# Performance work log

Hardware: AMD Instinct MI355X
Metric: run time of the kernel (lower is better)

The kernel has to match this reference:

```python
import jax, jax.numpy as jnp
import numpy as np

V, E, H2, TAG = 32000, 128, 256, 9
H = H2 // 2          # per-direction LSTM hidden
B, T = 128, 512


def setup_inputs() -> dict:
    key = jax.random.key(0)
    ks = jax.random.split(key, 15)
    s = 0.08
    n = lambda k, shp: jax.random.normal(k, shp, dtype=jnp.float32) * s
    return {
        "sentence": jax.random.randint(ks[0], (B, T), 0, V, dtype=jnp.int32),
        "tags": jax.random.randint(ks[1], (B, T), 0, TAG, dtype=jnp.int32),
        "mask": jnp.ones((B, T), dtype=bool),
        "embedding": n(ks[2], (V, E)),
        "w_ih_f": n(ks[3], (4 * H, E)),
        "w_hh_f": n(ks[4], (4 * H, H)),
        "b_f": n(ks[5], (4 * H,)),
        "w_ih_b": n(ks[6], (4 * H, E)),
        "w_hh_b": n(ks[7], (4 * H, H)),
        "b_b": n(ks[8], (4 * H,)),
        "w_out": n(ks[9], (TAG, H2)),
        "b_out": n(ks[10], (TAG,)),
        "start_trans": n(ks[11], (TAG,)),
        "end_trans": n(ks[12], (TAG,)),
        "trans": n(ks[13], (TAG, TAG)),
    }


def _lstm_dir(xp, w_hh):
    """xp: [T,B,4H] precomputed input projections (incl. bias). Returns h seq [T,B,H]."""
    Hn = w_hh.shape[1]
    Bn = xp.shape[1]

    def step(carry, x_t):
        h, c = carry
        g = x_t + h @ w_hh.T                       # [B,4H]
        i, f, gg, o = jnp.split(g, 4, axis=-1)     # torch gate order: i,f,g,o
        c = jax.nn.sigmoid(f) * c + jax.nn.sigmoid(i) * jnp.tanh(gg)
        h = jax.nn.sigmoid(o) * jnp.tanh(c)
        return (h, c), h

    init = (jnp.zeros((Bn, Hn), xp.dtype), jnp.zeros((Bn, Hn), xp.dtype))
    _, hs = jax.lax.scan(step, init, xp)
    return hs


def reference(sentence, tags, mask, embedding, w_ih_f, w_hh_f, b_f,
              w_ih_b, w_hh_b, b_b, w_out, b_out, start_trans, end_trans, trans):
    # ---- BiLSTM emissions ----
    x = embedding[sentence]                 # [B,T,E]
    xt = jnp.swapaxes(x, 0, 1)              # [T,B,E]
    h_f = _lstm_dir(xt @ w_ih_f.T + b_f, w_hh_f)                 # [T,B,H]
    h_b = _lstm_dir((xt @ w_ih_b.T + b_b)[::-1], w_hh_b)[::-1]   # [T,B,H]
    hcat = jnp.concatenate([h_f, h_b], axis=-1)                  # [T,B,2H]
    emissions = hcat @ w_out.T + b_out                           # [T,B,TAG]

    m = mask.T.astype(emissions.dtype)      # [T,B]
    tt = tags.T                             # [T,B]
    bidx = jnp.arange(tt.shape[1])

    # ---- CRF numerator (score of gold path), torchcrf semantics ----
    num0 = start_trans[tt[0]] + emissions[0, bidx, tt[0]]        # [B]

    def num_step(score, inp):
        e_t, t_prev, t_cur, m_t = inp
        return score + (trans[t_prev, t_cur] + e_t[bidx, t_cur]) * m_t, None

    num, _ = jax.lax.scan(num_step, num0, (emissions[1:], tt[:-1], tt[1:], m[1:]))
    seq_ends = mask.sum(axis=1).astype(jnp.int32) - 1            # [B]
    last_tags = tt[seq_ends, bidx]
    num = num + end_trans[last_tags]

    # ---- CRF log-partition (forward algorithm) ----
    alpha0 = start_trans + emissions[0]                          # [B,TAG]

    def fwd_step(alpha, inp):
        e_t, m_t = inp
        nxt = jax.nn.logsumexp(alpha[:, :, None] + trans[None] + e_t[:, None, :], axis=1)
        return jnp.where(m_t[:, None] > 0, nxt, alpha), None

    alpha, _ = jax.lax.scan(fwd_step, alpha0, (emissions[1:], m[1:]))
    logZ = jax.nn.logsumexp(alpha + end_trans, axis=1)           # [B]

    # forward returns -crf(...) with reduction='mean' => mean negative log-likelihood
    return -jnp.mean(num - logZ)
```

## Files before the change

kernel.cpp:

```cpp
#include <hip/hip_runtime.h>
#include <hip/hip_bf16.h>
#include <cstdint>
#include <cstddef>

#define NB   128
#define NT   512
#define NE   128
#define NH   128
#define NG   512
#define NTAG 9

typedef __bf16 bf16;
typedef __bf16 bf16x4 __attribute__((ext_vector_type(4)));
typedef __bf16 bf16x8 __attribute__((ext_vector_type(8)));
typedef _Float16 f16;
typedef _Float16 f16x2 __attribute__((ext_vector_type(2)));
typedef _Float16 f16x8 __attribute__((ext_vector_type(8)));
typedef float  floatx4 __attribute__((ext_vector_type(4)));

__device__ __forceinline__ float bflo_f32(unsigned u) {
  union { unsigned x; float f; } c; c.x = u << 16; return c.f;
}
__device__ __forceinline__ float bfhi_f32(unsigned u) {
  union { unsigned x; float f; } c; c.x = u & 0xFFFF0000u; return c.f;
}
__device__ __forceinline__ f16x2 pkh(float a, float b) {
  return __builtin_bit_cast(f16x2, __builtin_amdgcn_cvt_pkrtz(a, b));
}
__device__ __forceinline__ void block_sync_lds() {
  asm volatile("s_waitcnt lgkmcnt(0)\n\ts_barrier" ::: "memory");
}

__device__ __forceinline__ f16x2 sigm_h(f16x2 x) {
  const f16x2 lo = {(f16)(-2.5f), (f16)(-2.5f)}, hi = {(f16)2.5f, (f16)2.5f};
  x = __builtin_elementwise_min(__builtin_elementwise_max(x, lo), hi);
  f16x2 t = x * x;
  f16x2 p = t * (f16)0.0010154f + (f16)(-0.019144f);
  p = t * p + (f16)0.24964f;
  return x * p + (f16)0.5f;
}
__device__ __forceinline__ f16x2 tanh_h(f16x2 x) {
  const f16x2 lo = {(f16)(-1.5f), (f16)(-1.5f)}, hi = {(f16)1.5f, (f16)1.5f};
  x = __builtin_elementwise_min(__builtin_elementwise_max(x, lo), hi);
  f16x2 t = x * x;
  f16x2 p = t * (f16)0.045172f + (f16)(-0.27334f);
  p = t * p + (f16)0.98976f;
  return x * p;
}

__global__ __launch_bounds__(256, 1) void k_xp(
    const int* __restrict__ sentence, const float* __restrict__ emb,
    const float* __restrict__ w_ih_f, const float* __restrict__ w_ih_b,
    const float* __restrict__ b_f, const float* __restrict__ b_b,
    bf16* __restrict__ xp_f, bf16* __restrict__ xp_b)
{
  __shared__ bf16 Cld[128 * 136];
  const int t = blockIdx.x;
  const int tid = threadIdx.x;
  const int wv = tid >> 6, lane = tid & 63;
  const int lrow = lane & 15, quad = lane >> 4;
  const int m0 = (wv & 1) * 64, n0 = (wv >> 1) * 64;

  int tokv[4];
  #pragma unroll
  for (int mt = 0; mt < 4; ++mt)
    tokv[mt] = sentence[(size_t)(m0 + mt * 16 + lrow) * NT + t];

  bf16x8 af[4][4];
  #pragma unroll
  for (int kk = 0; kk < 4; ++kk)
    #pragma unroll
    for (int mt = 0; mt < 4; ++mt) {
      const float* s = emb + (size_t)tokv[mt] * NE + kk * 32 + quad * 8;
      float4 lo = *(const float4*)s;
      float4 hi = *(const float4*)(s + 4);
      bf16x8 v;
      v[0] = (bf16)lo.x; v[1] = (bf16)lo.y; v[2] = (bf16)lo.z; v[3] = (bf16)lo.w;
      v[4] = (bf16)hi.x; v[5] = (bf16)hi.y; v[6] = (bf16)hi.z; v[7] = (bf16)hi.w;
      af[kk][mt] = v;
    }

  bool first = true;
  #pragma unroll
  for (int d = 0; d < 2; ++d) {
    const float* Wd       = d ? w_ih_b : w_ih_f;
    const float* biasbase = d ? b_b  : b_f;
    bf16* outdir          = d ? xp_b : xp_f;
    for (int nb = 0; nb < 4; ++nb) {
      const int colbase = nb * 128;

      floatx4 acc[4][4] = {};
      #pragma unroll
      for (int kk = 0; kk < 4; ++kk) {
        bf16x8 bfr[4];
        #pragma unroll
        for (int nt = 0; nt < 4; ++nt) {
          const float* s = Wd + (size_t)(colbase + n0 + nt * 16 + lrow) * 128 + kk * 32 + quad * 8;
          float4 lo = *(const float4*)s;
          float4 hi = *(const float4*)(s + 4);
          bf16x8 v;
          v[0] = (bf16)lo.x; v[1] = (bf16)lo.y; v[2] = (bf16)lo.z; v[3] = (bf16)lo.w;
          v[4] = (bf16)hi.x; v[5] = (bf16)hi.y; v[6] = (bf16)hi.z; v[7] = (bf16)hi.w;
          bfr[nt] = v;
        }
        #pragma unroll
        for (int mt = 0; mt < 4; ++mt)
          #pragma unroll
          for (int nt = 0; nt < 4; ++nt)
            acc[mt][nt] = __builtin_amdgcn_mfma_f32_16x16x32_bf16(af[kk][mt], bfr[nt], acc[mt][nt], 0, 0, 0);
      }
      float bv[4];
      #pragma unroll
      for (int nt = 0; nt < 4; ++nt) bv[nt] = biasbase[colbase + n0 + nt * 16 + lrow];

      if (!first) __syncthreads();
      first = false;
      #pragma unroll
      for (int mt = 0; mt < 4; ++mt)
        #pragma unroll
        for (int nt = 0; nt < 4; ++nt) {
          bf16x4 v4;
          #pragma unroll
          for (int rr = 0; rr < 4; ++rr) v4[rr] = (bf16)(acc[mt][nt][rr] + bv[nt]);
          *(bf16x4*)&Cld[(n0 + nt * 16 + lrow) * 136 + m0 + mt * 16 + quad * 4] = v4;
        }
      __syncthreads();
      bf16* outbase = outdir + ((size_t)t * 8) * (512 * 16) + (size_t)colbase * 16;
      #pragma unroll
      for (int it = 0; it < 8; ++it) {
        const int p = it * 256 + tid;
        const int bg = p >> 8, n = (p >> 1) & 127, half = p & 1;
        *(bf16x8*)(outbase + ((size_t)bg * 512 + n) * 16 + half * 8) =
            *(const bf16x8*)&Cld[n * 136 + bg * 16 + half * 8];
      }
    }
  }
}

#define LSTM_STEP(PX, RB, WB)                                                  \
  do {                                                                         \
    f16x8 af[4];                                                               \
    _Pragma("unroll")                                                          \
    for (int kk = 0; kk < 4; ++kk)                                             \
      af[kk] = *(const f16x8*)&(RB)[lane * 8 + kk * 512];                      \
    floatx4 acc[4];                                                            \
    _Pragma("unroll")                                                          \
    for (int g = 0; g < 4; ++g) {                                              \
      acc[g][0] = bflo_f32(PX[g][0]); acc[g][1] = bfhi_f32(PX[g][0]);          \
      acc[g][2] = bflo_f32(PX[g][1]); acc[g][3] = bfhi_f32(PX[g][1]);          \
    }                                                                          \
    _Pragma("unroll")                                                          \
    for (int g = 0; g < 4; ++g) {             \
      uint2 u = *(const uint2*)pg[g];                                          \
      PX[g][0] = u.x; PX[g][1] = u.y;                                          \
      pg[g] += dstep_x;                                                        \
    }                                                                          \
    _Pragma("unroll")                                                          \
    for (int kk = 0; kk < 4; ++kk)                                             \
      _Pragma("unroll")                                                        \
      for (int g = 0; g < 4; ++g)                                              \
        acc[g] = __builtin_amdgcn_mfma_f32_16x16x32_f16(af[kk], wf[g][kk],     \
                                                        acc[g], 0, 0, 0);      \
    {                                                                          \
      f16x2 iv, fv, gv, ov, h2;                                                \
      iv = sigm_h(pkh(acc[0][0], acc[0][1]));                                  \
      fv = sigm_h(pkh(acc[1][0], acc[1][1]));                                  \
      gv = tanh_h(pkh(acc[2][0], acc[2][1]));                                  \
      ov = sigm_h(pkh(acc[3][0], acc[3][1]));                                  \
      c01 = fv * c01 + iv * gv;                                                \
      h2 = ov * tanh_h(c01);                                                   \
      (WB)[wboff + 0 * 8] = h2[0]; (WB)[wboff + 1 * 8] = h2[1];                \
      hop[0 * NH] = h2[0]; hop[1 * NH] = h2[1];                                \
      iv = sigm_h(pkh(acc[0][2], acc[0][3]));                                  \
      fv = sigm_h(pkh(acc[1][2], acc[1][3]));                                  \
      gv = tanh_h(pkh(acc[2][2], acc[2][3]));                                  \
      ov = sigm_h(pkh(acc[3][2], acc[3][3]));                                  \
      c23 = fv * c23 + iv * gv;                                                \
      h2 = ov * tanh_h(c23);                                                   \
      (WB)[wboff + 2 * 8] = h2[0]; (WB)[wboff + 3 * 8] = h2[1];                \
      hop[2 * NH] = h2[0]; hop[3 * NH] = h2[1];                                \
    }                                                                          \
    hop += dstep_h;                                                            \
    block_sync_lds();                                                          \
  } while (0)

__global__ __launch_bounds__(512, 1) void k_lstm(
    const bf16* __restrict__ xp_f, const bf16* __restrict__ xp_b,
    const float* __restrict__ w_hh_f, const float* __restrict__ w_hh_b,
    f16* __restrict__ h_f, f16* __restrict__ h_b)
{
  __shared__ f16 hfrag[2][2048];
  const int wg = blockIdx.x;
  const int dir = wg >> 3;
  const int bb = wg & 7;
  const int b0 = bb * 16;
  const bf16* __restrict__ xp   = dir ? xp_b   : xp_f;
  const float* __restrict__ Whh = dir ? w_hh_b : w_hh_f;
  f16* __restrict__ hout        = dir ? h_b    : h_f;
  const int tid = threadIdx.x;
  const int wv = tid >> 6, lane = tid & 63;
  const int lrow = lane & 15, quad = lane >> 4;
  const int hc = wv * 16 + lrow;

  f16x8 wf[4][4];
  #pragma unroll
  for (int g = 0; g < 4; ++g)
    #pragma unroll
    for (int kk = 0; kk < 4; ++kk) {
      const float* src = Whh + (size_t)(g * 128 + hc) * 128 + kk * 32 + quad * 8;
      f16x8 v;
      #pragma unroll
      for (int j = 0; j < 8; ++j) v[j] = (f16)src[j];
      wf[g][kk] = v;
    }
  {
    f16x2 z = {(f16)0.f, (f16)0.f};
    *(f16x2*)&hfrag[0][tid * 2] = z;
    *(f16x2*)&hfrag[0][1024 + tid * 2] = z;
  }

  const int t0 = dir ? (NT - 1) : 0;
  const ptrdiff_t dstep_x = dir ? -(ptrdiff_t)(8 * 512 * 16) : (ptrdiff_t)(8 * 512 * 16);
  const ptrdiff_t dstep_h = dir ? -(ptrdiff_t)(NB * NH) : (ptrdiff_t)(NB * NH);

  const bf16* pg[4];
  unsigned pxA[4][2], pxB[4][2];
  #pragma unroll
  for (int g = 0; g < 4; ++g)
    pg[g] = xp + (((size_t)t0 * 8 + bb) * 512 + g * 128 + hc) * 16 + quad * 4;
  #pragma unroll
  for (int g = 0; g < 4; ++g) {
    uint2 u = *(const uint2*)pg[g];
    pxA[g][0] = u.x; pxA[g][1] = u.y;
    pg[g] += dstep_x;
  }
  #pragma unroll
  for (int g = 0; g < 4; ++g) {
    uint2 u = *(const uint2*)pg[g];
    pxB[g][0] = u.x; pxB[g][1] = u.y;
    pg[g] += dstep_x;
  }
  f16* hop = hout + ((size_t)t0 * NB + b0 + quad * 4) * NH + hc;
  const int wboff = ((hc >> 3) * 16 + quad * 4) * 8 + (hc & 7);
  f16x2 c01 = {(f16)0.f, (f16)0.f}, c23 = {(f16)0.f, (f16)0.f};
  block_sync_lds();

  for (int s = 0; s < NT; s += 2) {
    LSTM_STEP(pxA, hfrag[0], hfrag[1]);
    LSTM_STEP(pxB, hfrag[1], hfrag[0]);
  }
}

__global__ __launch_bounds__(256, 1) void k_emis(
    const f16* __restrict__ h_f, const f16* __restrict__ h_b,
    const float* __restrict__ w_out, const float* __restrict__ b_out,
    float* __restrict__ emis, int* __restrict__ cnt_all)
{
  const int tid = threadIdx.x;
  if (blockIdx.x == 0 && tid == 0) *cnt_all = 0;
  const int wv = tid >> 6, lane = tid & 63;
  const int lrow = lane & 15, quad = lane >> 4;
  const int m0 = blockIdx.x * 64 + wv * 16;
  const size_t mrow = (size_t)(m0 + lrow);

  f16x8 wo[8];
  #pragma unroll
  for (int kk = 0; kk < 8; ++kk) {
    f16x8 v;
    #pragma unroll
    for (int j = 0; j < 8; ++j) v[j] = (f16)0.0f;
    if (lrow < NTAG) {
      const float* src = w_out + (size_t)lrow * 256 + kk * 32 + quad * 8;
      #pragma unroll
      for (int j = 0; j < 8; ++j) v[j] = (f16)src[j];
    }
    wo[kk] = v;
  }
  floatx4 acc = {};
  #pragma unroll
  for (int kk = 0; kk < 4; ++kk) {
    const f16x8 a = *(const f16x8*)&h_f[mrow * NH + kk * 32 + quad * 8];
    acc = __builtin_amdgcn_mfma_f32_16x16x32_f16(a, wo[kk], acc, 0, 0, 0);
  }
  #pragma unroll
  for (int kk = 0; kk < 4; ++kk) {
    const f16x8 a = *(const f16x8*)&h_b[mrow * NH + kk * 32 + quad * 8];
    acc = __builtin_amdgcn_mfma_f32_16x16x32_f16(a, wo[kk + 4], acc, 0, 0, 0);
  }
  if (lrow < NTAG) {
    const float bb = b_out[lrow];
    #pragma unroll
    for (int rr = 0; rr < 4; ++rr)
      emis[(size_t)(m0 + quad * 4 + rr) * NTAG + lrow] = acc[rr] + bb;
  }
}

__global__ __launch_bounds__(576, 1) void k_crf(
    const float* __restrict__ emis, const float* __restrict__ trans,
    const int* __restrict__ tags, const float* __restrict__ start_trans,
    const float* __restrict__ end_trans, float* __restrict__ res,
    int* __restrict__ cnt_all, float* __restrict__ out)
{
  __shared__ float Pl[64 * 81];
  __shared__ float nred[8];
  __shared__ int s_last;
  const int b = blockIdx.x;
  const int tid = threadIdx.x;

  float T[81];
  #pragma unroll
  for (int k = 0; k < 81; ++k) T[k] = trans[k];

  {
    const int c = tid / 9;
    const int i = tid - c * 9;
    const int t1 = 1 + 8 * c;
    const int nst = (c == 63) ? 6 : 7;
    const float* erow = emis + ((size_t)t1 * NB + b) * NTAG;
    float alpha[9];
    #pragma unroll
    for (int j = 0; j < 9; ++j) alpha[j] = trans[i * 9 + j] + erow[j];
    for (int tt = 0; tt < nst; ++tt) {
      erow += NB * NTAG;
      float e[9];
      #pragma unroll
      for (int j = 0; j < 9; ++j) e[j] = erow[j];
      float na[9];
      #pragma unroll
      for (int j = 0; j < 9; ++j) {
        float m = alpha[0] + T[0 * 9 + j];
        #pragma unroll
        for (int k = 1; k < 9; ++k) m = fmaxf(m, alpha[k] + T[k * 9 + j]);
        float s = 0.0f;
        #pragma unroll
        for (int k = 0; k < 9; ++k) s += __expf(alpha[k] + T[k * 9 + j] - m);
        na[j] = m + __logf(s) + e[j];
      }
      #pragma unroll
      for (int j = 0; j < 9; ++j) alpha[j] = na[j];
    }
    #pragma unroll
    for (int j = 0; j < 9; ++j) Pl[c * 81 + i * 9 + j] = alpha[j];
  }

  if (tid < 512) {
    float nval;
    if (tid == 0) {
      const int tg0 = tags[b * NT];
      const int tgl = tags[b * NT + NT - 1];
      nval = start_trans[tg0] + emis[b * NTAG + tg0] + end_trans[tgl];
    } else {
      const int tp = tags[b * NT + tid - 1];
      const int tc = tags[b * NT + tid];
      nval = trans[tp * NTAG + tc] + emis[(tid * NB + b) * NTAG + tc];
    }
    #pragma unroll
    for (int m = 32; m >= 1; m >>= 1) nval += __shfl_xor(nval, m, 64);
    if ((tid & 63) == 0) nred[tid >> 6] = nval;
  }
  __syncthreads();

  #pragma unroll
  for (int sp = 1; sp < 64; sp <<= 1) {
    const int nprod = 32 / sp;
    if (tid < nprod * 9) {
      const int p = tid / 9, i2 = tid - p * 9;
      const int c0 = p * 2 * sp;
      float Arow[9];
      #pragma unroll
      for (int k = 0; k < 9; ++k) Arow[k] = Pl[c0 * 81 + i2 * 9 + k];
      const float* Bm = &Pl[(c0 + sp) * 81];
      float Crow[9];
      #pragma unroll
      for (int j = 0; j < 9; ++j) {
        float m = Arow[0] + Bm[0 * 9 + j];
        #pragma unroll
        for (int k = 1; k < 9; ++k) m = fmaxf(m, Arow[k] + Bm[k * 9 + j]);
        float s = 0.0f;
        #pragma unroll
        for (int k = 0; k < 9; ++k) s += __expf(Arow[k] + Bm[k * 9 + j] - m);
        Crow[j] = m + __logf(s);
      }
      #pragma unroll
      for (int j = 0; j < 9; ++j) Pl[c0 * 81 + i2 * 9 + j] = Crow[j];
    }
    __syncthreads();
  }

  if (tid == 0) {
    float a0[9];
    #pragma unroll
    for (int j = 0; j < 9; ++j) a0[j] = start_trans[j] + emis[b * NTAG + j];
    float av[9];
    #pragma unroll
    for (int j = 0; j < 9; ++j) {
      float m = a0[0] + Pl[0 * 9 + j];
      #pragma unroll
      for (int k = 1; k < 9; ++k) m = fmaxf(m, a0[k] + Pl[k * 9 + j]);
      float s = 0.0f;
      #pragma unroll
      for (int k = 0; k < 9; ++k) s += __expf(a0[k] + Pl[k * 9 + j] - m);
      av[j] = m + __logf(s) + end_trans[j];
    }
    float m2 = av[0];
    #pragma unroll
    for (int k = 1; k < 9; ++k) m2 = fmaxf(m2, av[k]);
    float s2 = 0.0f;
    #pragma unroll
    for (int k = 0; k < 9; ++k) s2 += __expf(av[k] - m2);
    const float logZ = m2 + __logf(s2);
    float nsum = 0.0f;
    #pragma unroll
    for (int w = 0; w < 8; ++w) nsum += nred[w];
    res[b] = logZ - nsum;
  }

  if (tid == 0) {
    __threadfence();
    s_last = (atomicAdd(cnt_all, 1) == NB - 1) ? 1 : 0;
  }
  __syncthreads();
  if (!s_last) return;
  __threadfence();
  if (tid < 128) {
    float v = res[tid];
    #pragma unroll
    for (int m = 32; m >= 1; m >>= 1) v += __shfl_xor(v, m, 64);
    if ((tid & 63) == 0) nred[tid >> 6] = v;
  }
  __syncthreads();
  if (tid == 0) out[0] = (nred[0] + nred[1]) * (1.0f / 128.0f);
}

extern "C" void kernel_launch(void* const* d_in, const int* in_sizes, int n_in,
                              void* d_out, int out_size, void* d_ws, size_t ws_size,
                              hipStream_t stream)
{
  (void)in_sizes; (void)n_in; (void)out_size; (void)ws_size;
  const int*   sentence    = (const int*)d_in[0];
  const int*   tags        = (const int*)d_in[1];
  const float* embedding   = (const float*)d_in[3];
  const float* w_ih_f      = (const float*)d_in[4];
  const float* w_hh_f      = (const float*)d_in[5];
  const float* b_f         = (const float*)d_in[6];
  const float* w_ih_b      = (const float*)d_in[7];
  const float* w_hh_b      = (const float*)d_in[8];
  const float* b_b         = (const float*)d_in[9];
  const float* w_out       = (const float*)d_in[10];
  const float* b_out       = (const float*)d_in[11];
  const float* start_trans = (const float*)d_in[12];
  const float* end_trans   = (const float*)d_in[13];
  const float* trans       = (const float*)d_in[14];
  float* out = (float*)d_out;

  char* ws = (char*)d_ws;
  bf16*  xp_f = (bf16*)(ws);
  bf16*  xp_b = (bf16*)(ws + 67108864);
  f16*   h_f  = (f16*)(ws + 134217728);
  f16*   h_b  = (f16*)(ws + 150994944);
  float* emis = (float*)(ws + 167772160);
  float* res   = (float*)(ws + 136871936);
  int*   cnt_all = (int*)(ws);

  k_xp<<<512, 256, 0, stream>>>(sentence, embedding, w_ih_f, w_ih_b,
                                b_f, b_b, xp_f, xp_b);
  k_lstm<<<16, 512, 0, stream>>>(xp_f, xp_b, w_hh_f, w_hh_b, h_f, h_b);
  k_emis<<<1024, 256, 0, stream>>>(h_f, h_b, w_out, b_out, emis, cnt_all);
  k_crf<<<128, 576, 0, stream>>>(emis, trans, tags, start_trans, end_trans,
                                 res, cnt_all, out);
}
```

Baseline: 564.5 us.

## Fuse emission projection into CRF kernel with per-batch emissions in LDS

Removes the separate emission kernel. Each CRF block now computes its own batch row's emissions with MFMA from the LSTM hidden states and stores them in shared memory, instead of reading them from a global buffer. The counter reset moves to the xp kernel and the workspace offsets are rearranged. This saves a kernel launch and a global round trip for the emissions. In exchange, the CRF blocks take on strided hidden-state reads spread over only 128 blocks, and the larger shared-memory footprint may limit occupancy.

```diff
diff --git a/kernel.cpp b/kernel.cpp
--- a/kernel.cpp
+++ b/kernel.cpp
@@ -52,11 +52,12 @@
     const int* __restrict__ sentence, const float* __restrict__ emb,
     const float* __restrict__ w_ih_f, const float* __restrict__ w_ih_b,
     const float* __restrict__ b_f, const float* __restrict__ b_b,
-    bf16* __restrict__ xp_f, bf16* __restrict__ xp_b)
+    bf16* __restrict__ xp_f, bf16* __restrict__ xp_b, int* __restrict__ cnt_all)
 {
   __shared__ bf16 Cld[128 * 136];
   const int t = blockIdx.x;
   const int tid = threadIdx.x;
+  if (t == 0 && tid == 0) *cnt_all = 0;
   const int wv = tid >> 6, lane = tid & 63;
   const int lrow = lane & 15, quad = lane >> 4;
   const int m0 = (wv & 1) * 64, n0 = (wv >> 1) * 64;
@@ -251,61 +252,58 @@
   }
 }
 
-__global__ __launch_bounds__(256, 1) void k_emis(
+__global__ __launch_bounds__(576, 1) void k_crf(
     const f16* __restrict__ h_f, const f16* __restrict__ h_b,
     const float* __restrict__ w_out, const float* __restrict__ b_out,
-    float* __restrict__ emis, int* __restrict__ cnt_all)
+    const float* __restrict__ trans, const int* __restrict__ tags,
+    const float* __restrict__ start_trans, const float* __restrict__ end_trans,
+    float* __restrict__ res, int* __restrict__ cnt_all, float* __restrict__ out)
 {
-  const int tid = threadIdx.x;
-  if (blockIdx.x == 0 && tid == 0) *cnt_all = 0;
-  const int wv = tid >> 6, lane = tid & 63;
-  const int lrow = lane & 15, quad = lane >> 4;
-  const int m0 = blockIdx.x * 64 + wv * 16;
-  const size_t mrow = (size_t)(m0 + lrow);
-
-  f16x8 wo[8];
-  #pragma unroll
-  for (int kk = 0; kk < 8; ++kk) {
-    f16x8 v;
-    #pragma unroll
-    for (int j = 0; j < 8; ++j) v[j] = (f16)0.0f;
-    if (lrow < NTAG) {
-      const float* src = w_out + (size_t)lrow * 256 + kk * 32 + quad * 8;
-      #pragma unroll
-      for (int j = 0; j < 8; ++j) v[j] = (f16)src[j];
-    }
-    wo[kk] = v;
-  }
-  floatx4 acc = {};
-  #pragma unroll
-  for (int kk = 0; kk < 4; ++kk) {
-    const f16x8 a = *(const f16x8*)&h_f[mrow * NH + kk * 32 + quad * 8];
-    acc = __builtin_amdgcn_mfma_f32_16x16x32_f16(a, wo[kk], acc, 0, 0, 0);
-  }
-  #pragma unroll
-  for (int kk = 0; kk < 4; ++kk) {
-    const f16x8 a = *(const f16x8*)&h_b[mrow * NH + kk * 32 + quad * 8];
-    acc = __builtin_amdgcn_mfma_f32_16x16x32_f16(a, wo[kk + 4], acc, 0, 0, 0);
-  }
-  if (lrow < NTAG) {
-    const float bb = b_out[lrow];
-    #pragma unroll
-    for (int rr = 0; rr < 4; ++rr)
-      emis[(size_t)(m0 + quad * 4 + rr) * NTAG + lrow] = acc[rr] + bb;
-  }
-}
-
-__global__ __launch_bounds__(576, 1) void k_crf(
-    const float* __restrict__ emis, const float* __restrict__ trans,
-    const int* __restrict__ tags, const float* __restrict__ start_trans,
-    const float* __restrict__ end_trans, float* __restrict__ res,
-    int* __restrict__ cnt_all, float* __restrict__ out)
-{
+  __shared__ float emisL[NT * NTAG];
   __shared__ float Pl[64 * 81];
   __shared__ float nred[8];
   __shared__ int s_last;
   const int b = blockIdx.x;
   const int tid = threadIdx.x;
+  const int wv = tid >> 6, lane = tid & 63;
+  const int lrow = lane & 15, quad = lane >> 4;
+
+  {
+    f16x8 wo[8];
+    #pragma unroll
+    for (int kk = 0; kk < 8; ++kk) {
+      f16x8 v;
+      #pragma unroll
+      for (int j = 0; j < 8; ++j) v[j] = (f16)0.0f;
+      if (lrow < NTAG) {
+        const float* src = w_out + (size_t)lrow * 256 + kk * 32 + quad * 8;
+        #pragma unroll
+        for (int j = 0; j < 8; ++j) v[j] = (f16)src[j];
+      }
+      wo[kk] = v;
+    }
+    const float bo = (lrow < NTAG) ? b_out[lrow] : 0.0f;
+    for (int tile = wv; tile < 32; tile += 9) {
+      floatx4 acc = {};
+      const size_t arow = ((size_t)(tile * 16 + lrow) * NB + b) * NH;
+      #pragma unroll
+      for (int kk = 0; kk < 4; ++kk) {
+        const f16x8 a = *(const f16x8*)&h_f[arow + kk * 32 + quad * 8];
+        acc = __builtin_amdgcn_mfma_f32_16x16x32_f16(a, wo[kk], acc, 0, 0, 0);
+      }
+      #pragma unroll
+      for (int kk = 0; kk < 4; ++kk) {
+        const f16x8 a = *(const f16x8*)&h_b[arow + kk * 32 + quad * 8];
+        acc = __builtin_amdgcn_mfma_f32_16x16x32_f16(a, wo[kk + 4], acc, 0, 0, 0);
+      }
+      if (lrow < NTAG) {
+        #pragma unroll
+        for (int rr = 0; rr < 4; ++rr)
+          emisL[(tile * 16 + quad * 4 + rr) * NTAG + lrow] = acc[rr] + bo;
+      }
+    }
+  }
+  __syncthreads();
 
   float T[81];
   #pragma unroll
@@ -316,12 +314,12 @@
     const int i = tid - c * 9;
     const int t1 = 1 + 8 * c;
     const int nst = (c == 63) ? 6 : 7;
-    const float* erow = emis + ((size_t)t1 * NB + b) * NTAG;
+    const float* erow = &emisL[t1 * NTAG];
     float alpha[9];
     #pragma unroll
     for (int j = 0; j < 9; ++j) alpha[j] = trans[i * 9 + j] + erow[j];
     for (int tt = 0; tt < nst; ++tt) {
-      erow += NB * NTAG;
+      erow += NTAG;
       float e[9];
       #pragma unroll
       for (int j = 0; j < 9; ++j) e[j] = erow[j];
@@ -348,11 +346,11 @@
     if (tid == 0) {
       const int tg0 = tags[b * NT];
       const int tgl = tags[b * NT + NT - 1];
-      nval = start_trans[tg0] + emis[b * NTAG + tg0] + end_trans[tgl];
+      nval = start_trans[tg0] + emisL[tg0] + end_trans[tgl];
     } else {
       const int tp = tags[b * NT + tid - 1];
       const int tc = tags[b * NT + tid];
-      nval = trans[tp * NTAG + tc] + emis[(tid * NB + b) * NTAG + tc];
+      nval = trans[tp * NTAG + tc] + emisL[tid * NTAG + tc];
     }
     #pragma unroll
     for (int m = 32; m >= 1; m >>= 1) nval += __shfl_xor(nval, m, 64);
@@ -390,7 +388,7 @@
   if (tid == 0) {
     float a0[9];
     #pragma unroll
-    for (int j = 0; j < 9; ++j) a0[j] = start_trans[j] + emis[b * NTAG + j];
+    for (int j = 0; j < 9; ++j) a0[j] = start_trans[j] + emisL[j];
     float av[9];
     #pragma unroll
     for (int j = 0; j < 9; ++j) {
@@ -458,14 +456,12 @@
   bf16*  xp_b = (bf16*)(ws + 67108864);
   f16*   h_f  = (f16*)(ws + 134217728);
   f16*   h_b  = (f16*)(ws + 150994944);
-  float* emis = (float*)(ws + 167772160);
-  float* res   = (float*)(ws + 136871936);
-  int*   cnt_all = (int*)(ws);
+  int*   cnt_all = (int*)(ws + 167772160);
+  float* res     = (float*)(ws + 167772160 + 64);
 
   k_xp<<<512, 256, 0, stream>>>(sentence, embedding, w_ih_f, w_ih_b,
-                                b_f, b_b, xp_f, xp_b);
+                                b_f, b_b, xp_f, xp_b, cnt_all);
   k_lstm<<<16, 512, 0, stream>>>(xp_f, xp_b, w_hh_f, w_hh_b, h_f, h_b);
-  k_emis<<<1024, 256, 0, stream>>>(h_f, h_b, w_out, b_out, emis, cnt_all);
-  k_crf<<<128, 576, 0, stream>>>(emis, trans, tags, start_trans, end_trans,
-                                 res, cnt_all, out);
-}
+  k_crf<<<128, 576, 0, stream>>>(h_f, h_b, w_out, b_out, trans, tags,
+                                 start_trans, end_trans, res, cnt_all, out);
+}
```

Measured after the change: 565.7 us. About the same (+0.2%).
